# Kernel optimization log

Measured on AMD Instinct MI355X. Metric: run time of the kernel, lower is better.

The kernel has to match this reference:

```python
import jax, jax.numpy as jnp
import numpy as np

N_NODES = 100000
N_EDGES = 312500
D_IN = 256
D_HID = 256
D_OUT = 1


def setup_inputs() -> dict:
    key = jax.random.key(0)
    k_z, k_e, k_w1, k_b1, k_w2, k_b2 = jax.random.split(key, 6)
    z = jax.random.normal(k_z, (N_NODES, D_IN), dtype=jnp.float32)
    edge = jax.random.randint(k_e, (2, N_EDGES), 0, N_NODES, dtype=jnp.int64)
    # PyTorch Linear: y = x @ W.T + b; store W as [out, in]
    lim1 = 1.0 / np.sqrt(D_IN)
    W1 = jax.random.uniform(k_w1, (D_HID, D_IN), jnp.float32, -lim1, lim1)
    b1 = jax.random.uniform(k_b1, (D_HID,), jnp.float32, -lim1, lim1)
    lim2 = 1.0 / np.sqrt(D_HID)
    W2 = jax.random.uniform(k_w2, (D_OUT, D_HID), jnp.float32, -lim2, lim2)
    b2 = jax.random.uniform(k_b2, (D_OUT,), jnp.float32, -lim2, lim2)
    return {"z": z, "edge": edge, "W1": W1, "b1": b1, "W2": W2, "b2": b2}


def reference(z, edge, W1, b1, W2, b2):
    # gather endpoint embeddings and multiply elementwise: [E, D_IN]
    x = z[edge[0]] * z[edge[1]]
    # dropout is identity in eval mode
    x = jnp.einsum('ed,hd->eh', x, W1) + b1  # [E, D_HID]
    x = jax.nn.elu(x)
    x = jnp.einsum('eh,oh->eo', x, W2) + b2  # [E, 1]
    return x
```

## Files before the change

### kernel.cpp

```cpp
#include <hip/hip_runtime.h>
#include <hip/hip_bf16.h>

#define N_EDGES 312500
#define N_NODES 100000
#define D 256
#define BM 256
#define TILES (BM / 32)

typedef __attribute__((ext_vector_type(8)))  short bf16x8;
typedef __attribute__((ext_vector_type(16))) float f32x16;

static __device__ __forceinline__ unsigned short f2bf(float f) {
    union { float f; unsigned u; } c; c.f = f;
    unsigned r = c.u + 0x7fffu + ((c.u >> 16) & 1u);
    return (unsigned short)(r >> 16);
}

__global__ void prep_w1(const float* __restrict__ W1, unsigned short* __restrict__ packed) {
    int t = blockIdx.x * blockDim.x + threadIdx.x;
    if (t >= 8192) return;
    int lane = t & 63;
    int ktnt = t >> 6;
    int kt = ktnt & 15;
    int nt = ktnt >> 4;
    int r  = nt * 32 + (lane & 31);
    int c0 = kt * 16 + (lane >> 5) * 8;
    const float* src = W1 + r * D + c0;
    unsigned short v[8];
#pragma unroll
    for (int j = 0; j < 8; ++j) v[j] = f2bf(src[j]);
    uint4 u;
    u.x = (unsigned)v[0] | ((unsigned)v[1] << 16);
    u.y = (unsigned)v[2] | ((unsigned)v[3] << 16);
    u.z = (unsigned)v[4] | ((unsigned)v[5] << 16);
    u.w = (unsigned)v[6] | ((unsigned)v[7] << 16);
    reinterpret_cast<uint4*>(packed)[t] = u;
}

__global__ void prep_z(const float* __restrict__ z, unsigned short* __restrict__ zb) {
    int t = blockIdx.x * blockDim.x + threadIdx.x;
    if (t >= (N_NODES * D) / 8) return;
    const float4* src = reinterpret_cast<const float4*>(z) + 2 * (size_t)t;
    float4 v0 = src[0], v1 = src[1];
    uint4 u;
    u.x = (unsigned)f2bf(v0.x) | ((unsigned)f2bf(v0.y) << 16);
    u.y = (unsigned)f2bf(v0.z) | ((unsigned)f2bf(v0.w) << 16);
    u.z = (unsigned)f2bf(v1.x) | ((unsigned)f2bf(v1.y) << 16);
    u.w = (unsigned)f2bf(v1.z) | ((unsigned)f2bf(v1.w) << 16);
    reinterpret_cast<uint4*>(zb)[t] = u;
}

template<bool ZB>
__global__ __launch_bounds__(512, 4) void edge_decoder(
    const float* __restrict__ z,
    const unsigned short* __restrict__ zb,
    const int* __restrict__ edge,
    const unsigned short* __restrict__ w1p,
    const float* __restrict__ b1,
    const float* __restrict__ W2,
    const float* __restrict__ b2,
    float* __restrict__ out)
{
    __shared__ unsigned char ldsT[2][16 * 64 * 16];
    __shared__ float  sbufp[TILES][8][32];
    __shared__ float2 epi[8][2][16];
    __shared__ int    lidx[2][BM];

    const int tid  = threadIdx.x;
    const int lane = tid & 63;
    const int w    = tid >> 6;
    const int blockBase = blockIdx.x * BM;

    const int gkt  = lane >> 2;
    const int gkh  = (lane >> 1) & 1;
    const int ghal = lane & 1;
    const int d0   = 4 * lane;
    const int gktx = gkt & 7;

    bf16x8 a[16];
    {
        const bf16x8* bp = reinterpret_cast<const bf16x8*>(w1p);
#pragma unroll
        for (int kt = 0; kt < 16; ++kt)
            a[kt] = bp[(w * 16 + kt) * 64 + lane];
    }
    {
        int e = blockBase + (tid & 255);
        if (e >= N_EDGES) e = N_EDGES - 1;
        int half = tid >> 8;
        lidx[half][tid & 255] = edge[half * N_EDGES + e];
    }
    if (tid < 256) {
        int w_  = tid >> 5;
        int kh_ = (tid >> 4) & 1;
        int r_  = tid & 15;
        int h   = w_ * 32 + (r_ & 3) + 8 * (r_ >> 2) + 4 * kh_;
        epi[w_][kh_][r_] = make_float2(b1[h], W2[h]);
    }
    __syncthreads();

    uint2 P[4], Q[4];
    auto issue = [&](int t) {
#pragma unroll
        for (int j = 0; j < 4; ++j) {
            int el = t * 32 + w * 4 + j;
            int i0 = lidx[0][el];
            int i1 = lidx[1][el];
            P[j] = *reinterpret_cast<const uint2*>(zb + (size_t)i0 * D + d0);
            Q[j] = *reinterpret_cast<const uint2*>(zb + (size_t)i1 * D + d0);
        }
    };
    auto commit = [&](int b) {
        unsigned char* tb = ldsT[b] + (gkt << 10);
#pragma unroll
        for (int j = 0; j < 4; ++j) {
            __hip_bfloat162 h0 = __hmul2(*reinterpret_cast<const __hip_bfloat162*>(&P[j].x),
                                         *reinterpret_cast<const __hip_bfloat162*>(&Q[j].x));
            __hip_bfloat162 h1 = __hmul2(*reinterpret_cast<const __hip_bfloat162*>(&P[j].y),
                                         *reinterpret_cast<const __hip_bfloat162*>(&Q[j].y));
            int m = w * 4 + j;
            int unit = (m + (gkh << 5)) ^ gktx;
            *reinterpret_cast<uint2*>(tb + unit * 16 + ghal * 8) =
                make_uint2(*reinterpret_cast<unsigned*>(&h0),
                           *reinterpret_cast<unsigned*>(&h1));
        }
    };
    auto stage_serial = [&](int t, int b) {
        unsigned char* tb = ldsT[b] + (gkt << 10);
#pragma unroll
        for (int j = 0; j < 4; ++j) {
            int el = t * 32 + w * 4 + j;
            int i0 = lidx[0][el];
            int i1 = lidx[1][el];
            float4 p = *reinterpret_cast<const float4*>(z + (size_t)i0 * D + d0);
            float4 q = *reinterpret_cast<const float4*>(z + (size_t)i1 * D + d0);
            __hip_bfloat162 h0 = __float22bfloat162_rn(make_float2(p.x * q.x, p.y * q.y));
            __hip_bfloat162 h1 = __float22bfloat162_rn(make_float2(p.z * q.z, p.w * q.w));
            int m = w * 4 + j;
            int unit = (m + (gkh << 5)) ^ gktx;
            *reinterpret_cast<uint2*>(tb + unit * 16 + ghal * 8) =
                make_uint2(*reinterpret_cast<unsigned*>(&h0),
                           *reinterpret_cast<unsigned*>(&h1));
        }
    };

    if constexpr (ZB) { issue(0); commit(0); }
    else              { stage_serial(0, 0); }
    __syncthreads();

    const int kh = lane >> 5;

#pragma unroll 1
    for (int t = 0; t < TILES; ++t) {
        if constexpr (ZB) { if (t + 1 < TILES) issue(t + 1); }

        const unsigned char* tb = ldsT[t & 1];
        f32x16 acc;
#pragma unroll
        for (int i = 0; i < 16; ++i) acc[i] = 0.f;
#pragma unroll
        for (int kt = 0; kt < 16; ++kt) {
            bf16x8 bfrag = *reinterpret_cast<const bf16x8*>(
                tb + (kt << 10) + ((lane ^ (kt & 7)) << 4));
            acc = __builtin_amdgcn_mfma_f32_32x32x16_bf16(a[kt], bfrag, acc, 0, 0, 0);
        }

        float s = 0.f;
#pragma unroll
        for (int r = 0; r < 16; ++r) {
            float2 bw = epi[w][kh][r];
            float h = acc[r] + bw.x;
            s += (h > 0.f ? h : (__expf(h) - 1.0f)) * bw.y;
        }
        s += __shfl_xor(s, 32);
        if (lane < 32) sbufp[t][w][lane] = s;

        if constexpr (ZB) { if (t + 1 < TILES) commit((t + 1) & 1); }
        else              { if (t + 1 < TILES) stage_serial(t + 1, (t + 1) & 1); }

        __syncthreads();
    }

    if (tid < BM) {
        int t  = tid >> 5;
        int e  = tid & 31;
        float sum = b2[0];
#pragma unroll
        for (int ww = 0; ww < 8; ++ww) sum += sbufp[t][ww][e];
        int eo = blockBase + tid;
        if (eo < N_EDGES) out[eo] = sum;
    }
}

extern "C" void kernel_launch(void* const* d_in, const int* in_sizes, int n_in,
                              void* d_out, int out_size, void* d_ws, size_t ws_size,
                              hipStream_t stream) {
    const float* z    = (const float*)d_in[0];
    const int*   edge = (const int*)d_in[1];
    const float* W1   = (const float*)d_in[2];
    const float* b1   = (const float*)d_in[3];
    const float* W2   = (const float*)d_in[4];
    const float* b2   = (const float*)d_in[5];
    float*       out  = (float*)d_out;

    unsigned short* w1p = (unsigned short*)d_ws;
    const size_t zbOff  = 131072;
    const size_t zbNeed = zbOff + (size_t)N_NODES * D * 2;

    prep_w1<<<32, 256, 0, stream>>>(W1, w1p);

    int blocks = (N_EDGES + BM - 1) / BM;
    if (ws_size >= zbNeed) {
        unsigned short* zb = (unsigned short*)((char*)d_ws + zbOff);
        prep_z<<<(N_NODES * D / 8 + 255) / 256, 256, 0, stream>>>(z, zb);
        edge_decoder<true><<<blocks, 512, 0, stream>>>(z, zb, edge, w1p, b1, W2, b2, out);
    } else {
        edge_decoder<false><<<blocks, 512, 0, stream>>>(z, nullptr, edge, w1p, b1, W2, b2, out);
    }
}
```

Baseline: 96.03 us.

## Deepen gather prefetch to two tiles ahead with double register sets

Restructures the tile loop to unroll by two and keep two sets of gathered z rows in registers (A and B), so global gathers are issued two tiles ahead of their commit to LDS instead of one. This gives the random-access loads more time to complete behind MFMA work. It doubles the register footprint for the prefetched data, which may pressure occupancy under the 512x4 launch bound.

```diff
diff --git a/kernel.cpp b/kernel.cpp
--- a/kernel.cpp
+++ b/kernel.cpp
@@ -99,25 +99,31 @@
     }
     __syncthreads();
 
-    uint2 P[4], Q[4];
-    auto issue = [&](int t) {
+    uint2 PA[4], QA[4], PB[4], QB[4];
+    auto issueA = [&](int t) {
 #pragma unroll
         for (int j = 0; j < 4; ++j) {
             int el = t * 32 + w * 4 + j;
-            int i0 = lidx[0][el];
-            int i1 = lidx[1][el];
-            P[j] = *reinterpret_cast<const uint2*>(zb + (size_t)i0 * D + d0);
-            Q[j] = *reinterpret_cast<const uint2*>(zb + (size_t)i1 * D + d0);
-        }
-    };
-    auto commit = [&](int b) {
-        unsigned char* tb = ldsT[b] + (gkt << 10);
-#pragma unroll
-        for (int j = 0; j < 4; ++j) {
-            __hip_bfloat162 h0 = __hmul2(*reinterpret_cast<const __hip_bfloat162*>(&P[j].x),
-                                         *reinterpret_cast<const __hip_bfloat162*>(&Q[j].x));
-            __hip_bfloat162 h1 = __hmul2(*reinterpret_cast<const __hip_bfloat162*>(&P[j].y),
-                                         *reinterpret_cast<const __hip_bfloat162*>(&Q[j].y));
+            PA[j] = *reinterpret_cast<const uint2*>(zb + (size_t)lidx[0][el] * D + d0);
+            QA[j] = *reinterpret_cast<const uint2*>(zb + (size_t)lidx[1][el] * D + d0);
+        }
+    };
+    auto issueB = [&](int t) {
+#pragma unroll
+        for (int j = 0; j < 4; ++j) {
+            int el = t * 32 + w * 4 + j;
+            PB[j] = *reinterpret_cast<const uint2*>(zb + (size_t)lidx[0][el] * D + d0);
+            QB[j] = *reinterpret_cast<const uint2*>(zb + (size_t)lidx[1][el] * D + d0);
+        }
+    };
+    auto commitA = [&]() {
+        unsigned char* tb = ldsT[0] + (gkt << 10);
+#pragma unroll
+        for (int j = 0; j < 4; ++j) {
+            __hip_bfloat162 h0 = __hmul2(*reinterpret_cast<const __hip_bfloat162*>(&PA[j].x),
+                                         *reinterpret_cast<const __hip_bfloat162*>(&QA[j].x));
+            __hip_bfloat162 h1 = __hmul2(*reinterpret_cast<const __hip_bfloat162*>(&PA[j].y),
+                                         *reinterpret_cast<const __hip_bfloat162*>(&QA[j].y));
             int m = w * 4 + j;
             int unit = (m + (gkh << 5)) ^ gktx;
             *reinterpret_cast<uint2*>(tb + unit * 16 + ghal * 8) =
@@ -125,15 +131,28 @@
                            *reinterpret_cast<unsigned*>(&h1));
         }
     };
+    auto commitB = [&]() {
+        unsigned char* tb = ldsT[1] + (gkt << 10);
+#pragma unroll
+        for (int j = 0; j < 4; ++j) {
+            __hip_bfloat162 h0 = __hmul2(*reinterpret_cast<const __hip_bfloat162*>(&PB[j].x),
+                                         *reinterpret_cast<const __hip_bfloat162*>(&QB[j].x));
+            __hip_bfloat162 h1 = __hmul2(*reinterpret_cast<const __hip_bfloat162*>(&PB[j].y),
+                                         *reinterpret_cast<const __hip_bfloat162*>(&QB[j].y));
+            int m = w * 4 + j;
+            int unit = (m + (gkh << 5)) ^ gktx;
+            *reinterpret_cast<uint2*>(tb + unit * 16 + ghal * 8) =
+                make_uint2(*reinterpret_cast<unsigned*>(&h0),
+                           *reinterpret_cast<unsigned*>(&h1));
+        }
+    };
     auto stage_serial = [&](int t, int b) {
         unsigned char* tb = ldsT[b] + (gkt << 10);
 #pragma unroll
         for (int j = 0; j < 4; ++j) {
             int el = t * 32 + w * 4 + j;
-            int i0 = lidx[0][el];
-            int i1 = lidx[1][el];
-            float4 p = *reinterpret_cast<const float4*>(z + (size_t)i0 * D + d0);
-            float4 q = *reinterpret_cast<const float4*>(z + (size_t)i1 * D + d0);
+            float4 p = *reinterpret_cast<const float4*>(z + (size_t)lidx[0][el] * D + d0);
+            float4 q = *reinterpret_cast<const float4*>(z + (size_t)lidx[1][el] * D + d0);
             __hip_bfloat162 h0 = __float22bfloat162_rn(make_float2(p.x * q.x, p.y * q.y));
             __hip_bfloat162 h1 = __float22bfloat162_rn(make_float2(p.z * q.z, p.w * q.w));
             int m = w * 4 + j;
@@ -144,17 +163,9 @@
         }
     };
 
-    if constexpr (ZB) { issue(0); commit(0); }
-    else              { stage_serial(0, 0); }
-    __syncthreads();
-
     const int kh = lane >> 5;
 
-#pragma unroll 1
-    for (int t = 0; t < TILES; ++t) {
-        if constexpr (ZB) { if (t + 1 < TILES) issue(t + 1); }
-
-        const unsigned char* tb = ldsT[t & 1];
+    auto compute_tile = [&](int t, const unsigned char* tb) {
         f32x16 acc;
 #pragma unroll
         for (int i = 0; i < 16; ++i) acc[i] = 0.f;
@@ -164,7 +175,6 @@
                 tb + (kt << 10) + ((lane ^ (kt & 7)) << 4));
             acc = __builtin_amdgcn_mfma_f32_32x32x16_bf16(a[kt], bfrag, acc, 0, 0, 0);
         }
-
         float s = 0.f;
 #pragma unroll
         for (int r = 0; r < 16; ++r) {
@@ -174,10 +184,23 @@
         }
         s += __shfl_xor(s, 32);
         if (lane < 32) sbufp[t][w][lane] = s;
-
-        if constexpr (ZB) { if (t + 1 < TILES) commit((t + 1) & 1); }
-        else              { if (t + 1 < TILES) stage_serial(t + 1, (t + 1) & 1); }
-
+    };
+
+    if constexpr (ZB) { issueA(0); issueB(1); commitA(); }
+    else              { stage_serial(0, 0); }
+    __syncthreads();
+
+#pragma unroll 1
+    for (int t = 0; t < TILES; t += 2) {
+        if constexpr (ZB) { if (t + 2 < TILES) issueA(t + 2); }
+        compute_tile(t, ldsT[0]);
+        if constexpr (ZB) { commitB(); }
+        else              { stage_serial(t + 1, 1); }
+        __syncthreads();
+        if constexpr (ZB) { if (t + 3 < TILES) issueB(t + 3); }
+        compute_tile(t + 1, ldsT[1]);
+        if constexpr (ZB) { if (t + 2 < TILES) commitA(); }
+        else              { if (t + 2 < TILES) stage_serial(t + 2, 0); }
         __syncthreads();
     }
 
```

New measurement: 162.6 us. +69.4%, slower.
